# Optimization experiments

Hardware: AMD Instinct MI355X
Metric: run time of the kernel (lower is better)

The kernel has to match this reference:

```python
import jax, jax.numpy as jnp
import numpy as np
from jax import lax

B, T_ENC, T_DEC, F = 64, 1024, 256, 8
U = 256          # enc_units == dec_units
H, D = 8, 32     # num_heads * key_dim == U (residual constraint)
EPS = 1e-5


def layer_norm(x, g, b):
    m = jnp.mean(x, axis=-1, keepdims=True)
    v = jnp.mean(jnp.square(x - m), axis=-1, keepdims=True)
    return g * (x - m) / jnp.sqrt(v + EPS) + b


def lstm_scan(x, W, Urec, bias, h0, c0):
    # x: [B,T,F]; keras gate order i,f,g,o
    def step(carry, xt):
        h, c = carry
        z = xt @ W + h @ Urec + bias
        i, f, g, o = jnp.split(z, 4, axis=-1)
        c = jax.nn.sigmoid(f) * c + jax.nn.sigmoid(i) * jnp.tanh(g)
        h = jax.nn.sigmoid(o) * jnp.tanh(c)
        return (h, c), h
    (h, c), hs = lax.scan(step, (h0, c0), jnp.swapaxes(x, 0, 1))
    return jnp.swapaxes(hs, 0, 1), h, c


def mha(q_in, kv_in, Wq, bq, Wk, bk, Wv, bv, Wo, bo):
    Bq, Tq = q_in.shape[0], q_in.shape[1]
    Tk = kv_in.shape[1]
    q = (q_in @ Wq + bq).reshape(Bq, Tq, H, D).transpose(0, 2, 1, 3)
    k = (kv_in @ Wk + bk).reshape(Bq, Tk, H, D).transpose(0, 2, 1, 3)
    v = (kv_in @ Wv + bv).reshape(Bq, Tk, H, D).transpose(0, 2, 1, 3)
    scores = jnp.einsum('bhqd,bhkd->bhqk', q, k) * (D ** -0.5)
    w = jax.nn.softmax(scores, axis=-1)
    ctx = jnp.einsum('bhqk,bhkd->bhqd', w, v)
    ctx = ctx.transpose(0, 2, 1, 3).reshape(Bq, Tq, H * D)
    return ctx @ Wo + bo


def setup_inputs() -> dict:
    key = jax.random.key(0)
    ks = jax.random.split(key, 24)
    g = lambda k, s: (jax.random.normal(k, s, dtype=jnp.float32) * 0.05)
    return {
        'enc_in': jax.random.normal(ks[0], (B, T_ENC, F), dtype=jnp.float32),
        'dec_in': jax.random.normal(ks[1], (B, T_DEC, F), dtype=jnp.float32),
        'ln_enc_g': jnp.ones((F,), jnp.float32), 'ln_enc_b': jnp.zeros((F,), jnp.float32),
        'W_enc': g(ks[2], (F, 4 * U)), 'U_enc': g(ks[3], (U, 4 * U)), 'b_enc': jnp.zeros((4 * U,), jnp.float32),
        'W_dec': g(ks[4], (F, 4 * U)), 'U_dec': g(ks[5], (U, 4 * U)), 'b_dec': jnp.zeros((4 * U,), jnp.float32),
        'Wq': g(ks[6], (U, H * D)), 'bq': jnp.zeros((H * D,), jnp.float32),
        'Wk': g(ks[7], (U, H * D)), 'bk': jnp.zeros((H * D,), jnp.float32),
        'Wv': g(ks[8], (U, H * D)), 'bv': jnp.zeros((H * D,), jnp.float32),
        'Wo': g(ks[9], (H * D, H * D)), 'bo': jnp.zeros((H * D,), jnp.float32),
        'ln_post_g': jnp.ones((U,), jnp.float32), 'ln_post_b': jnp.zeros((U,), jnp.float32),
        'W_out': g(ks[10], (U, 1)), 'b_out': jnp.zeros((1,), jnp.float32),
    }


def reference(enc_in, dec_in, ln_enc_g, ln_enc_b, W_enc, U_enc, b_enc,
              W_dec, U_dec, b_dec, Wq, bq, Wk, bk, Wv, bv, Wo, bo,
              ln_post_g, ln_post_b, W_out, b_out):
    x = layer_norm(enc_in, ln_enc_g, ln_enc_b)
    h0 = jnp.zeros((enc_in.shape[0], U), enc_in.dtype)
    c0 = jnp.zeros((enc_in.shape[0], U), enc_in.dtype)
    enc_seq, h, c = lstm_scan(x, W_enc, U_enc, b_enc, h0, c0)
    dec_seq, _, _ = lstm_scan(dec_in, W_dec, U_dec, b_dec, h, c)
    ctx = mha(dec_seq, enc_seq, Wq, bq, Wk, bk, Wv, bv, Wo, bo)
    mix = layer_norm(dec_seq + ctx, ln_post_g, ln_post_b)
    return mix @ W_out + b_out
```

## Files before the change

kernel.cpp:

```cpp
#include <hip/hip_runtime.h>
#include <stdint.h>

#define NBATCH 64
#define TENC   1024
#define TDEC   256
#define FDIM   8
#define UDIM   256
#define GDIM   1024
#define NHEAD  8
#define DHEAD  32
#define LNEPS  1e-5f

#define KP_TOT 132
#define KP_W   33
#define KP_V   25
#define KP_L   8

typedef unsigned int   u32;
typedef unsigned short u16;

typedef _Float16 half2v __attribute__((ext_vector_type(2)));

__device__ __forceinline__ float bf2f_lo(u32 w) { return __uint_as_float(w << 16); }
__device__ __forceinline__ float bf2f_hi(u32 w) { return __uint_as_float(w & 0xFFFF0000u); }
__device__ __forceinline__ u16 f2bf(float f) {
  u32 u = __float_as_uint(f);
  u = (u + 0x7FFFu + ((u >> 16) & 1u)) >> 16;
  return (u16)u;
}
__device__ __forceinline__ u16 f2h_bits(float f) {
  _Float16 h = (_Float16)f;
  return __builtin_bit_cast(u16, h);
}
__device__ __forceinline__ float fdot2p(u32 wp, u32 hp, float acc) {
  return __builtin_amdgcn_fdot2(__builtin_bit_cast(half2v, wp),
                                __builtin_bit_cast(half2v, hp), acc, false);
}
__device__ __forceinline__ float sigf(float x) { return 1.0f / (1.0f + __expf(-x)); }
__device__ __forceinline__ float tanhf_fast(float x) {
  float ax = fabsf(x);
  float e  = __expf(2.0f * ax);
  float r  = 1.0f - 2.0f / (e + 1.0f);
  return copysignf(r, x);
}

__global__ __launch_bounds__(256)
void k_ln8(const float* __restrict__ x, const float* __restrict__ g,
           const float* __restrict__ bt, float* __restrict__ y, int rows) {
  int r = blockIdx.x * blockDim.x + threadIdx.x;
  if (r >= rows) return;
  const float* xp = x + (size_t)r * 8;
  float4 a = ((const float4*)xp)[0];
  float4 b4 = ((const float4*)xp)[1];
  float v[8] = {a.x, a.y, a.z, a.w, b4.x, b4.y, b4.z, b4.w};
  float m = 0.f;
#pragma unroll
  for (int i = 0; i < 8; ++i) m += v[i];
  m *= 0.125f;
  float var = 0.f;
#pragma unroll
  for (int i = 0; i < 8; ++i) { float d = v[i] - m; var += d * d; }
  var *= 0.125f;
  float rs = rsqrtf(var + LNEPS);
  float o[8];
#pragma unroll
  for (int i = 0; i < 8; ++i) o[i] = g[i] * (v[i] - m) * rs + bt[i];
  float* yp = y + (size_t)r * 8;
  ((float4*)yp)[0] = make_float4(o[0], o[1], o[2], o[3]);
  ((float4*)yp)[1] = make_float4(o[4], o[5], o[6], o[7]);
}

__global__ __launch_bounds__(256)
void k_packUW(const float* __restrict__ U, const float* __restrict__ W,
              u32* __restrict__ out) {
  int idx = blockIdx.x * 256 + threadIdx.x;
  if (idx >= KP_TOT * GDIM) return;
  int kp = idx >> 10, c = idx & 1023;
  int r0 = 2 * kp, r1 = 2 * kp + 1;
  float f0 = (r0 < 256) ? U[(size_t)r0 * GDIM + c] : W[(size_t)(r0 - 256) * GDIM + c];
  float f1 = (r1 < 256) ? U[(size_t)r1 * GDIM + c] : W[(size_t)(r1 - 256) * GDIM + c];
  out[idx] = (u32)f2h_bits(f0) | ((u32)f2h_bits(f1) << 16);
}

#define DOT4(w4, hh)                                              \
  do {                                                            \
    a0 = fdot2p((w4).x, (hh), a0); a1 = fdot2p((w4).y, (hh), a1); \
    a2 = fdot2p((w4).z, (hh), a2); a3 = fdot2p((w4).w, (hh), a3); \
  } while (0)

__global__ __launch_bounds__(1024, 1)
void k_scan2(const float* __restrict__ xseq,
             const u32* __restrict__ Upk,
             const float* __restrict__ bias,
             const float* __restrict__ h0, const float* __restrict__ c0,
             float* __restrict__ seq_out,
             float* __restrict__ hT, float* __restrict__ cT, int T) {
  __shared__ __align__(16) uint4 wl[1024 * KP_L];
  __shared__ __align__(16) float zp[4][1024];
  __shared__ __align__(16) u32  hpk[4][36];
  __shared__ __align__(16) float biasl[1024];

  const int tid = threadIdx.x, b = blockIdx.x;
  const int w = tid >> 6, lane = tid & 63;
  const int ks = w >> 2, cg = w & 3;
  const int c0i = cg * 256 + lane * 4;

  const uint4* up = (const uint4*)Upk;
  const int ubase = ks * KP_W * 256 + (c0i >> 2);
  uint4 wv[KP_V];
#pragma unroll
  for (int i = 0; i < KP_V; ++i) wv[i] = up[ubase + i * 256];
  for (int i = 0; i < KP_L; ++i)
    wl[(tid << 3) + (i ^ (lane & 7))] = up[ubase + (KP_V + i) * 256];
  biasl[tid] = bias[tid];

  const int m = tid >> 1;
  const int hks = (m >= 99) ? 3 : (m >= 66) ? 2 : (m >= 33) ? 1 : 0;
  const int hii = m - hks * KP_W;

  float c_reg = 0.f, h_last = 0.f;
  if (tid < 256) {
    float hv = h0 ? h0[b * 256 + tid] : 0.f;
    c_reg = c0 ? c0[b * 256 + tid] : 0.f;
    h_last = hv;
    ((u16*)&hpk[hks][hii])[tid & 1] = f2h_bits(hv);
  }
  if (tid < 8) {
    float xv = xseq[(size_t)(b * T + 0) * 8 + tid];
    ((u16*)&hpk[3][29 + (tid >> 1)])[tid & 1] = f2h_bits(xv);
  }
  __syncthreads();

  for (int t = 0; t < T; ++t) {
    const u32* hrow = &hpk[ks][0];
    float a0 = 0.f, a1 = 0.f, a2 = 0.f, a3 = 0.f;
#pragma unroll
    for (int ch = 0; ch < 6; ++ch) {
      uint4 hq = *(const uint4*)(hrow + ch * 4);
      DOT4(wv[ch * 4 + 0], hq.x);
      DOT4(wv[ch * 4 + 1], hq.y);
      DOT4(wv[ch * 4 + 2], hq.z);
      DOT4(wv[ch * 4 + 3], hq.w);
    }
    {
      u32 hh = hrow[24];
      DOT4(wv[24], hh);
    }
#pragma unroll
    for (int jj = 0; jj < KP_L; ++jj) {
      uint4 w4 = wl[(tid << 3) + (jj ^ (lane & 7))];
      u32 hh = hrow[KP_V + jj];
      DOT4(w4, hh);
    }
    *(float4*)&zp[ks][c0i] = make_float4(a0, a1, a2, a3);
    __syncthreads();

    if (tid < 256) {
      float zi = biasl[tid] + zp[0][tid] + zp[1][tid] + zp[2][tid] + zp[3][tid];
      float zf = biasl[256 + tid] + zp[0][256 + tid] + zp[1][256 + tid] +
                 zp[2][256 + tid] + zp[3][256 + tid];
      float zg = biasl[512 + tid] + zp[0][512 + tid] + zp[1][512 + tid] +
                 zp[2][512 + tid] + zp[3][512 + tid];
      float zo = biasl[768 + tid] + zp[0][768 + tid] + zp[1][768 + tid] +
                 zp[2][768 + tid] + zp[3][768 + tid];
      float ig = sigf(zi), fg = sigf(zf);
      float gg = tanhf_fast(zg), og = sigf(zo);
      c_reg = fg * c_reg + ig * gg;
      float h = og * tanhf_fast(c_reg);
      h_last = h;
      seq_out[(size_t)(b * T + t) * 256 + tid] = h;
      ((u16*)&hpk[hks][hii])[tid & 1] = f2h_bits(h);
    }
    if (tid < 8) {
      int t2 = (t + 1 < T) ? (t + 1) : (T - 1);
      float xv = xseq[(size_t)(b * T + t2) * 8 + tid];
      ((u16*)&hpk[3][29 + (tid >> 1)])[tid & 1] = f2h_bits(xv);
    }
    __syncthreads();
  }
  if (hT && tid < 256) {
    hT[b * 256 + tid] = h_last;
    cT[b * 256 + tid] = c_reg;
  }
}

template <int OMODE>
__global__ __launch_bounds__(256)
void k_gemm256(const float* __restrict__ A, const float* __restrict__ Bw,
               const float* __restrict__ bias, void* __restrict__ outp,
               int M, int Tdim) {
  __shared__ __align__(16) float As[16][68];
  __shared__ __align__(16) float Bs[16][68];
  const int tid = threadIdx.x;
  const int tx = tid & 15, ty = tid >> 4;
  const int bm = blockIdx.x * 64, bn = blockIdx.y * 64;
  const int ar = tid >> 2, ac = (tid & 3) << 2;
  const int br = tid >> 4, bc = (tid & 15) << 2;
  float acc[4][4] = {};
  for (int k0 = 0; k0 < 256; k0 += 16) {
    float4 av = *(const float4*)(A + (size_t)(bm + ar) * 256 + k0 + ac);
    As[ac + 0][ar] = av.x; As[ac + 1][ar] = av.y;
    As[ac + 2][ar] = av.z; As[ac + 3][ar] = av.w;
    float4 bv = *(const float4*)(Bw + (size_t)(k0 + br) * 256 + bn + bc);
    *(float4*)&Bs[br][bc] = bv;
    __syncthreads();
#pragma unroll
    for (int k = 0; k < 16; ++k) {
      float4 a4 = *(const float4*)&As[k][ty << 2];
      float4 b4 = *(const float4*)&Bs[k][tx << 2];
      float aa[4] = {a4.x, a4.y, a4.z, a4.w};
      float bb[4] = {b4.x, b4.y, b4.z, b4.w};
#pragma unroll
      for (int i = 0; i < 4; ++i)
#pragma unroll
        for (int jj = 0; jj < 4; ++jj)
          acc[i][jj] = fmaf(aa[i], bb[jj], acc[i][jj]);
    }
    __syncthreads();
  }
#pragma unroll
  for (int i = 0; i < 4; ++i) {
    int mm = bm + (ty << 2) + i;
#pragma unroll
    for (int jj = 0; jj < 4; ++jj) {
      int n = bn + (tx << 2) + jj;
      float v = acc[i][jj] + bias[n];
      if (OMODE == 0) {
        ((float*)outp)[(size_t)mm * 256 + n] = v;
      } else {
        int bb_ = mm / Tdim, t = mm % Tdim;
        int hh = n >> 5, dd = n & 31;
        size_t o = ((((size_t)bb_ * NHEAD + hh) * Tdim) + t) * 32 + dd;
        if (OMODE == 1) ((float*)outp)[o] = v;
        else            ((u16*)outp)[o]   = f2bf(v);
      }
    }
  }
}

__global__ __launch_bounds__(256)
void k_attn(const float* __restrict__ Q, const u16* __restrict__ Kb,
            const u16* __restrict__ Vb, float* __restrict__ ctx) {
  const int bh = blockIdx.x;
  const int b = bh >> 3, h = bh & 7;
  const int tid = threadIdx.x;
  __shared__ __align__(16) float Kl[64][36];
  __shared__ __align__(16) float Vl[64][36];
  float q[32];
  {
    const float* qp = Q + ((size_t)bh * TDEC + tid) * 32;
#pragma unroll
    for (int i = 0; i < 8; ++i) {
      float4 v = ((const float4*)qp)[i];
      q[i * 4 + 0] = v.x * 0.17677669529663687f;
      q[i * 4 + 1] = v.y * 0.17677669529663687f;
      q[i * 4 + 2] = v.z * 0.17677669529663687f;
      q[i * 4 + 3] = v.w * 0.17677669529663687f;
    }
  }
  float mrun = -3.0e38f, lrun = 0.f;
  float acc[32];
#pragma unroll
  for (int i = 0; i < 32; ++i) acc[i] = 0.f;
  const int lr = tid >> 2, lc = (tid & 3) << 3;
  for (int kt = 0; kt < TENC; kt += 64) {
    {
      uint4 kw = *(const uint4*)(Kb + ((size_t)bh * TENC + kt + lr) * 32 + lc);
      Kl[lr][lc + 0] = bf2f_lo(kw.x); Kl[lr][lc + 1] = bf2f_hi(kw.x);
      Kl[lr][lc + 2] = bf2f_lo(kw.y); Kl[lr][lc + 3] = bf2f_hi(kw.y);
      Kl[lr][lc + 4] = bf2f_lo(kw.z); Kl[lr][lc + 5] = bf2f_hi(kw.z);
      Kl[lr][lc + 6] = bf2f_lo(kw.w); Kl[lr][lc + 7] = bf2f_hi(kw.w);
      uint4 vw = *(const uint4*)(Vb + ((size_t)bh * TENC + kt + lr) * 32 + lc);
      Vl[lr][lc + 0] = bf2f_lo(vw.x); Vl[lr][lc + 1] = bf2f_hi(vw.x);
      Vl[lr][lc + 2] = bf2f_lo(vw.y); Vl[lr][lc + 3] = bf2f_hi(vw.y);
      Vl[lr][lc + 4] = bf2f_lo(vw.z); Vl[lr][lc + 5] = bf2f_hi(vw.z);
      Vl[lr][lc + 6] = bf2f_lo(vw.w); Vl[lr][lc + 7] = bf2f_hi(vw.w);
    }
    __syncthreads();
#pragma unroll
    for (int cch = 0; cch < 8; ++cch) {
      float s8[8];
#pragma unroll
      for (int i = 0; i < 8; ++i) {
        const float4* kr = (const float4*)&Kl[cch * 8 + i][0];
        float ss = 0.f;
#pragma unroll
        for (int d4 = 0; d4 < 8; ++d4) {
          float4 kv = kr[d4];
          ss = fmaf(q[d4 * 4 + 0], kv.x, ss);
          ss = fmaf(q[d4 * 4 + 1], kv.y, ss);
          ss = fmaf(q[d4 * 4 + 2], kv.z, ss);
          ss = fmaf(q[d4 * 4 + 3], kv.w, ss);
        }
        s8[i] = ss;
      }
      float mnew = mrun;
#pragma unroll
      for (int i = 0; i < 8; ++i) mnew = fmaxf(mnew, s8[i]);
      float sc = __expf(mrun - mnew);
      mrun = mnew;
      lrun *= sc;
#pragma unroll
      for (int d = 0; d < 32; ++d) acc[d] *= sc;
#pragma unroll
      for (int i = 0; i < 8; ++i) {
        float p = __expf(s8[i] - mnew);
        lrun += p;
        const float4* vr = (const float4*)&Vl[cch * 8 + i][0];
#pragma unroll
        for (int d4 = 0; d4 < 8; ++d4) {
          float4 vv = vr[d4];
          acc[d4 * 4 + 0] = fmaf(p, vv.x, acc[d4 * 4 + 0]);
          acc[d4 * 4 + 1] = fmaf(p, vv.y, acc[d4 * 4 + 1]);
          acc[d4 * 4 + 2] = fmaf(p, vv.z, acc[d4 * 4 + 2]);
          acc[d4 * 4 + 3] = fmaf(p, vv.w, acc[d4 * 4 + 3]);
        }
      }
    }
    __syncthreads();
  }
  float inv = 1.0f / lrun;
  float* op = ctx + ((size_t)(b * TDEC + tid) * 256 + h * 32);
#pragma unroll
  for (int i = 0; i < 8; ++i) {
    ((float4*)op)[i] = make_float4(acc[i * 4 + 0] * inv, acc[i * 4 + 1] * inv,
                                   acc[i * 4 + 2] * inv, acc[i * 4 + 3] * inv);
  }
}

__global__ __launch_bounds__(256)
void k_final(const float* __restrict__ dec_seq, const float* __restrict__ ctxo,
             const float* __restrict__ g, const float* __restrict__ bb,
             const float* __restrict__ Wout, const float* __restrict__ bout,
             float* __restrict__ out) {
  const int wv = threadIdx.x >> 6, lane = threadIdx.x & 63;
  const int row = blockIdx.x * 4 + wv;
  const size_t base = (size_t)row * 256 + lane * 4;
  float4 dv = *(const float4*)(dec_seq + base);
  float4 cv = *(const float4*)(ctxo + base);
  float v[4] = {dv.x + cv.x, dv.y + cv.y, dv.z + cv.z, dv.w + cv.w};
  float s = v[0] + v[1] + v[2] + v[3];
#pragma unroll
  for (int off = 32; off >= 1; off >>= 1) s += __shfl_xor(s, off, 64);
  float m = s * (1.0f / 256.0f);
  float d2 = 0.f;
#pragma unroll
  for (int i = 0; i < 4; ++i) { float d = v[i] - m; d2 += d * d; }
#pragma unroll
  for (int off = 32; off >= 1; off >>= 1) d2 += __shfl_xor(d2, off, 64);
  float rs = rsqrtf(d2 * (1.0f / 256.0f) + LNEPS);
  float4 g4 = *(const float4*)(g + lane * 4);
  float4 b4 = *(const float4*)(bb + lane * 4);
  float4 w4 = *(const float4*)(Wout + lane * 4);
  float mix0 = g4.x * (v[0] - m) * rs + b4.x;
  float mix1 = g4.y * (v[1] - m) * rs + b4.y;
  float mix2 = g4.z * (v[2] - m) * rs + b4.z;
  float mix3 = g4.w * (v[3] - m) * rs + b4.w;
  float p = mix0 * w4.x + mix1 * w4.y + mix2 * w4.z + mix3 * w4.w;
#pragma unroll
  for (int off = 32; off >= 1; off >>= 1) p += __shfl_xor(p, off, 64);
  if (lane == 0) out[row] = p + bout[0];
}

extern "C" void kernel_launch(void* const* d_in, const int* in_sizes, int n_in,
                              void* d_out, int out_size, void* d_ws, size_t ws_size,
                              hipStream_t stream) {
  const float* enc_in   = (const float*)d_in[0];
  const float* dec_in   = (const float*)d_in[1];
  const float* ln_enc_g = (const float*)d_in[2];
  const float* ln_enc_b = (const float*)d_in[3];
  const float* W_enc    = (const float*)d_in[4];
  const float* U_enc    = (const float*)d_in[5];
  const float* b_enc    = (const float*)d_in[6];
  const float* W_dec    = (const float*)d_in[7];
  const float* U_dec    = (const float*)d_in[8];
  const float* b_dec    = (const float*)d_in[9];
  const float* Wq = (const float*)d_in[10]; const float* bq = (const float*)d_in[11];
  const float* Wk = (const float*)d_in[12]; const float* bk = (const float*)d_in[13];
  const float* Wv = (const float*)d_in[14]; const float* bv = (const float*)d_in[15];
  const float* Wo = (const float*)d_in[16]; const float* bo = (const float*)d_in[17];
  const float* ln_post_g = (const float*)d_in[18];
  const float* ln_post_b = (const float*)d_in[19];
  const float* W_out     = (const float*)d_in[20];
  const float* b_out     = (const float*)d_in[21];

  char* ws = (char*)d_ws;
  size_t off = 0;
  auto alloc = [&](size_t bytes) -> void* {
    void* p = ws + off;
    off += (bytes + 255) & ~(size_t)255;
    return p;
  };
  float* xln     = (float*)alloc((size_t)NBATCH * TENC * 8 * 4);
  u32*   upkE    = (u32*)  alloc((size_t)KP_TOT * GDIM * 4);
  u32*   upkD    = (u32*)  alloc((size_t)KP_TOT * GDIM * 4);
  float* enc_seq = (float*)alloc((size_t)NBATCH * TENC * 256 * 4);
  float* dec_seq = (float*)alloc((size_t)NBATCH * TDEC * 256 * 4);
  float* hfin    = (float*)alloc((size_t)NBATCH * 256 * 4);
  float* cfin    = (float*)alloc((size_t)NBATCH * 256 * 4);
  float* Qp      = (float*)alloc((size_t)NBATCH * NHEAD * TDEC * 32 * 4);
  u16*   Kb      = (u16*)  alloc((size_t)NBATCH * NHEAD * TENC * 32 * 2);
  u16*   Vb      = (u16*)  alloc((size_t)NBATCH * NHEAD * TENC * 32 * 2);
  float* ctx     = (float*)alloc((size_t)NBATCH * TDEC * 256 * 4);
  float* ctxo    = (float*)alloc((size_t)NBATCH * TDEC * 256 * 4);

  k_ln8<<<dim3(256), dim3(256), 0, stream>>>(enc_in, ln_enc_g, ln_enc_b, xln,
                                             NBATCH * TENC);
  k_packUW<<<dim3((KP_TOT * GDIM + 255) / 256), dim3(256), 0, stream>>>(U_enc, W_enc, upkE);
  k_packUW<<<dim3((KP_TOT * GDIM + 255) / 256), dim3(256), 0, stream>>>(U_dec, W_dec, upkD);
  k_scan2<<<dim3(NBATCH), dim3(1024), 0, stream>>>(
      xln, upkE, b_enc, nullptr, nullptr, enc_seq, hfin, cfin, TENC);
  k_scan2<<<dim3(NBATCH), dim3(1024), 0, stream>>>(
      dec_in, upkD, b_dec, hfin, cfin, dec_seq, nullptr, nullptr, TDEC);
  k_gemm256<1><<<dim3(256, 4), dim3(256), 0, stream>>>(dec_seq, Wq, bq, Qp, NBATCH * TDEC, TDEC);
  k_gemm256<2><<<dim3(1024, 4), dim3(256), 0, stream>>>(enc_seq, Wk, bk, Kb, NBATCH * TENC, TENC);
  k_gemm256<2><<<dim3(1024, 4), dim3(256), 0, stream>>>(enc_seq, Wv, bv, Vb, NBATCH * TENC, TENC);
  k_attn<<<dim3(NBATCH * NHEAD), dim3(256), 0, stream>>>(Qp, Kb, Vb, ctx);
  k_gemm256<0><<<dim3(256, 4), dim3(256), 0, stream>>>(ctx, Wo, bo, ctxo, NBATCH * TDEC, 0x7fffffff);
  k_final<<<dim3(NBATCH * TDEC / 4), dim3(256), 0, stream>>>(
      dec_seq, ctxo, ln_post_g, ln_post_b, W_out, b_out, (float*)d_out);
}
```

Measured before the change: 3.450 ms.

## Interleave LSTM gate columns per unit so gate sums stay in registers

Repacks the recurrent and input weights so each thread owns the four gates (i,f,g,o) of one hidden unit instead of four adjacent columns of one gate. The k-split-0 threads keep their partial sums in registers, only three k-splits write float4 partials to shared memory, and bias is held in registers. The x prefetch load is hoisted to the start of the step on an otherwise idle thread. The register/LDS split moves from 25/8 to 24/9 uint4 rows and launch bounds change to (1024,4), which may alter register allocation and risk spills.

```diff
diff --git a/kernel.cpp b/kernel.cpp
--- a/kernel.cpp
+++ b/kernel.cpp
@@ -11,10 +11,9 @@
 #define DHEAD  32
 #define LNEPS  1e-5f
 
-#define KP_TOT 132
 #define KP_W   33
-#define KP_V   25
-#define KP_L   8
+#define KP_V   24
+#define KP_L   9
 
 typedef unsigned int   u32;
 typedef unsigned short u16;
@@ -71,15 +70,21 @@
 }
 
 __global__ __launch_bounds__(256)
-void k_packUW(const float* __restrict__ U, const float* __restrict__ W,
-              u32* __restrict__ out) {
+void k_packUW2(const float* __restrict__ U, const float* __restrict__ W,
+               uint4* __restrict__ out) {
   int idx = blockIdx.x * 256 + threadIdx.x;
-  if (idx >= KP_TOT * GDIM) return;
-  int kp = idx >> 10, c = idx & 1023;
-  int r0 = 2 * kp, r1 = 2 * kp + 1;
-  float f0 = (r0 < 256) ? U[(size_t)r0 * GDIM + c] : W[(size_t)(r0 - 256) * GDIM + c];
-  float f1 = (r1 < 256) ? U[(size_t)r1 * GDIM + c] : W[(size_t)(r1 - 256) * GDIM + c];
-  out[idx] = (u32)f2h_bits(f0) | ((u32)f2h_bits(f1) << 16);
+  int gp = idx >> 8, u = idx & 255;
+  int r0 = 2 * gp, r1 = 2 * gp + 1;
+  const float* R0 = (r0 < 256) ? (U + (size_t)r0 * GDIM) : (W + (size_t)(r0 - 256) * GDIM);
+  const float* R1 = (r1 < 256) ? (U + (size_t)r1 * GDIM) : (W + (size_t)(r1 - 256) * GDIM);
+  uint4 o;
+  u32* oc = (u32*)&o;
+#pragma unroll
+  for (int g = 0; g < 4; ++g) {
+    int c = g * 256 + u;
+    oc[g] = (u32)f2h_bits(R0[c]) | ((u32)f2h_bits(R1[c]) << 16);
+  }
+  out[idx] = o;
 }
 
 #define DOT4(w4, hh)                                              \
@@ -88,51 +93,59 @@
     a2 = fdot2p((w4).z, (hh), a2); a3 = fdot2p((w4).w, (hh), a3); \
   } while (0)
 
-__global__ __launch_bounds__(1024, 1)
-void k_scan2(const float* __restrict__ xseq,
-             const u32* __restrict__ Upk,
+__global__ __launch_bounds__(1024, 4)
+void k_scan3(const float* __restrict__ xseq,
+             const uint4* __restrict__ Wpk,
              const float* __restrict__ bias,
              const float* __restrict__ h0, const float* __restrict__ c0,
              float* __restrict__ seq_out,
              float* __restrict__ hT, float* __restrict__ cT, int T) {
-  __shared__ __align__(16) uint4 wl[1024 * KP_L];
-  __shared__ __align__(16) float zp[4][1024];
-  __shared__ __align__(16) u32  hpk[4][36];
-  __shared__ __align__(16) float biasl[1024];
+  __shared__ __align__(16) uint4  wl[1024 * KP_L];
+  __shared__ __align__(16) float4 zp[3 * 256];
+  __shared__ __align__(16) u32    hpk[4 * 36];
 
   const int tid = threadIdx.x, b = blockIdx.x;
   const int w = tid >> 6, lane = tid & 63;
   const int ks = w >> 2, cg = w & 3;
-  const int c0i = cg * 256 + lane * 4;
-
-  const uint4* up = (const uint4*)Upk;
-  const int ubase = ks * KP_W * 256 + (c0i >> 2);
+  const int u = cg * 64 + lane;
+
+  const int base = ks * KP_W * 256 + u;
   uint4 wv[KP_V];
 #pragma unroll
-  for (int i = 0; i < KP_V; ++i) wv[i] = up[ubase + i * 256];
-  for (int i = 0; i < KP_L; ++i)
-    wl[(tid << 3) + (i ^ (lane & 7))] = up[ubase + (KP_V + i) * 256];
-  biasl[tid] = bias[tid];
-
-  const int m = tid >> 1;
-  const int hks = (m >= 99) ? 3 : (m >= 66) ? 2 : (m >= 33) ? 1 : 0;
-  const int hii = m - hks * KP_W;
+  for (int i = 0; i < KP_V; ++i) wv[i] = Wpk[base + i * 256];
+  const int widx = tid * KP_L;
+#pragma unroll
+  for (int i = 0; i < KP_L; ++i) wl[widx + i] = Wpk[base + (KP_V + i) * 256];
+
+  const float bi = bias[u], bf = bias[256 + u], bg = bias[512 + u], bo = bias[768 + u];
+  const int m_ = u >> 1;
+  const int s_ = (m_ >= 99) ? 3 : (m_ >= 66) ? 2 : (m_ >= 33) ? 1 : 0;
+  const int hoff = (s_ * 36 + (m_ - s_ * 33)) * 2 + (u & 1);
+
+  const bool is_x = (tid >= 960 && tid < 968);
+  const int xj = tid - 960;
+  const int xoff = (3 * 36 + 29 + (xj >> 1)) * 2 + (xj & 1);
 
   float c_reg = 0.f, h_last = 0.f;
   if (tid < 256) {
-    float hv = h0 ? h0[b * 256 + tid] : 0.f;
-    c_reg = c0 ? c0[b * 256 + tid] : 0.f;
+    float hv = h0 ? h0[b * 256 + u] : 0.f;
+    c_reg = c0 ? c0[b * 256 + u] : 0.f;
     h_last = hv;
-    ((u16*)&hpk[hks][hii])[tid & 1] = f2h_bits(hv);
-  }
-  if (tid < 8) {
-    float xv = xseq[(size_t)(b * T + 0) * 8 + tid];
-    ((u16*)&hpk[3][29 + (tid >> 1)])[tid & 1] = f2h_bits(xv);
+    ((u16*)hpk)[hoff] = f2h_bits(hv);
+  }
+  if (is_x) {
+    float xv = xseq[(size_t)(b * T + 0) * 8 + xj];
+    ((u16*)hpk)[xoff] = f2h_bits(xv);
   }
   __syncthreads();
 
+  const u32* hrow = hpk + ks * 36;
   for (int t = 0; t < T; ++t) {
-    const u32* hrow = &hpk[ks][0];
+    float xv_next = 0.f;
+    if (is_x) {
+      int t2 = (t + 1 < T) ? (t + 1) : (T - 1);
+      xv_next = xseq[(size_t)(b * T + t2) * 8 + xj];
+    }
     float a0 = 0.f, a1 = 0.f, a2 = 0.f, a3 = 0.f;
 #pragma unroll
     for (int ch = 0; ch < 6; ++ch) {
@@ -143,44 +156,43 @@
       DOT4(wv[ch * 4 + 3], hq.w);
     }
     {
-      u32 hh = hrow[24];
-      DOT4(wv[24], hh);
-    }
-#pragma unroll
-    for (int jj = 0; jj < KP_L; ++jj) {
-      uint4 w4 = wl[(tid << 3) + (jj ^ (lane & 7))];
-      u32 hh = hrow[KP_V + jj];
-      DOT4(w4, hh);
-    }
-    *(float4*)&zp[ks][c0i] = make_float4(a0, a1, a2, a3);
+      uint4 hq6 = *(const uint4*)(hrow + 24);
+      uint4 hq7 = *(const uint4*)(hrow + 28);
+      u32 h32 = hrow[32];
+      uint4 w4;
+      w4 = wl[widx + 0]; DOT4(w4, hq6.x);
+      w4 = wl[widx + 1]; DOT4(w4, hq6.y);
+      w4 = wl[widx + 2]; DOT4(w4, hq6.z);
+      w4 = wl[widx + 3]; DOT4(w4, hq6.w);
+      w4 = wl[widx + 4]; DOT4(w4, hq7.x);
+      w4 = wl[widx + 5]; DOT4(w4, hq7.y);
+      w4 = wl[widx + 6]; DOT4(w4, hq7.z);
+      w4 = wl[widx + 7]; DOT4(w4, hq7.w);
+      w4 = wl[widx + 8]; DOT4(w4, h32);
+    }
+    if (ks) zp[(ks - 1) * 256 + u] = make_float4(a0, a1, a2, a3);
     __syncthreads();
 
     if (tid < 256) {
-      float zi = biasl[tid] + zp[0][tid] + zp[1][tid] + zp[2][tid] + zp[3][tid];
-      float zf = biasl[256 + tid] + zp[0][256 + tid] + zp[1][256 + tid] +
-                 zp[2][256 + tid] + zp[3][256 + tid];
-      float zg = biasl[512 + tid] + zp[0][512 + tid] + zp[1][512 + tid] +
-                 zp[2][512 + tid] + zp[3][512 + tid];
-      float zo = biasl[768 + tid] + zp[0][768 + tid] + zp[1][768 + tid] +
-                 zp[2][768 + tid] + zp[3][768 + tid];
+      float4 p1 = zp[u], p2 = zp[256 + u], p3 = zp[512 + u];
+      float zi = a0 + bi + p1.x + p2.x + p3.x;
+      float zf = a1 + bf + p1.y + p2.y + p3.y;
+      float zg = a2 + bg + p1.z + p2.z + p3.z;
+      float zo = a3 + bo + p1.w + p2.w + p3.w;
       float ig = sigf(zi), fg = sigf(zf);
       float gg = tanhf_fast(zg), og = sigf(zo);
       c_reg = fg * c_reg + ig * gg;
       float h = og * tanhf_fast(c_reg);
       h_last = h;
-      seq_out[(size_t)(b * T + t) * 256 + tid] = h;
-      ((u16*)&hpk[hks][hii])[tid & 1] = f2h_bits(h);
-    }
-    if (tid < 8) {
-      int t2 = (t + 1 < T) ? (t + 1) : (T - 1);
-      float xv = xseq[(size_t)(b * T + t2) * 8 + tid];
-      ((u16*)&hpk[3][29 + (tid >> 1)])[tid & 1] = f2h_bits(xv);
-    }
+      seq_out[(size_t)(b * T + t) * 256 + u] = h;
+      ((u16*)hpk)[hoff] = f2h_bits(h);
+    }
+    if (is_x) ((u16*)hpk)[xoff] = f2h_bits(xv_next);
     __syncthreads();
   }
   if (hT && tid < 256) {
-    hT[b * 256 + tid] = h_last;
-    cT[b * 256 + tid] = c_reg;
+    hT[b * 256 + u] = h_last;
+    cT[b * 256 + u] = c_reg;
   }
 }
 
@@ -392,8 +404,8 @@
     return p;
   };
   float* xln     = (float*)alloc((size_t)NBATCH * TENC * 8 * 4);
-  u32*   upkE    = (u32*)  alloc((size_t)KP_TOT * GDIM * 4);
-  u32*   upkD    = (u32*)  alloc((size_t)KP_TOT * GDIM * 4);
+  uint4* upkE    = (uint4*)alloc((size_t)132 * 256 * 16);
+  uint4* upkD    = (uint4*)alloc((size_t)132 * 256 * 16);
   float* enc_seq = (float*)alloc((size_t)NBATCH * TENC * 256 * 4);
   float* dec_seq = (float*)alloc((size_t)NBATCH * TDEC * 256 * 4);
   float* hfin    = (float*)alloc((size_t)NBATCH * 256 * 4);
@@ -406,11 +418,11 @@
 
   k_ln8<<<dim3(256), dim3(256), 0, stream>>>(enc_in, ln_enc_g, ln_enc_b, xln,
                                              NBATCH * TENC);
-  k_packUW<<<dim3((KP_TOT * GDIM + 255) / 256), dim3(256), 0, stream>>>(U_enc, W_enc, upkE);
-  k_packUW<<<dim3((KP_TOT * GDIM + 255) / 256), dim3(256), 0, stream>>>(U_dec, W_dec, upkD);
-  k_scan2<<<dim3(NBATCH), dim3(1024), 0, stream>>>(
+  k_packUW2<<<dim3(132), dim3(256), 0, stream>>>(U_enc, W_enc, upkE);
+  k_packUW2<<<dim3(132), dim3(256), 0, stream>>>(U_dec, W_dec, upkD);
+  k_scan3<<<dim3(NBATCH), dim3(1024), 0, stream>>>(
       xln, upkE, b_enc, nullptr, nullptr, enc_seq, hfin, cfin, TENC);
-  k_scan2<<<dim3(NBATCH), dim3(1024), 0, stream>>>(
+  k_scan3<<<dim3(NBATCH), dim3(1024), 0, stream>>>(
       dec_in, upkD, b_dec, hfin, cfin, dec_seq, nullptr, nullptr, TDEC);
   k_gemm256<1><<<dim3(256, 4), dim3(256), 0, stream>>>(dec_seq, Wq, bq, Qp, NBATCH * TDEC, TDEC);
   k_gemm256<2><<<dim3(1024, 4), dim3(256), 0, stream>>>(enc_seq, Wk, bk, Kb, NBATCH * TENC, TENC);
```

Result: faster. 3.357 ms (-2.7%).
